# Performance work log

Hardware: AMD Instinct MI355X
Metric: run time of the kernel (lower is better)

## Reference

```python
import jax, jax.numpy as jnp
from jax import lax
import numpy as np
import math

B, H, W = 4, 1080, 1080
MINSIZE = 20
FACTOR = 0.709
THRESH = 0.6
STRIDE = 2.0
CELL = 12.0


def get_scales():
    scales = []
    scale = CELL / MINSIZE
    m = scale * min(H, W)
    while m >= 12:
        scales.append(scale)
        scale *= FACTOR
        m *= FACTOR
    return scales


def setup_inputs() -> dict:
    key = jax.random.key(0)
    ks = jax.random.split(key, 6)
    init = lambda k, shp: jax.random.normal(k, shp, jnp.float32) * 0.1
    return {
        "inputs": jax.random.uniform(ks[0], (B, H, W, 3), jnp.float32) * 255.0,
        "w1": init(ks[1], (3, 3, 3, 10)), "b1": jnp.zeros((10,), jnp.float32),
        "w2": init(ks[2], (3, 3, 10, 16)), "b2": jnp.zeros((16,), jnp.float32),
        "w3": init(ks[3], (3, 3, 16, 32)), "b3": jnp.zeros((32,), jnp.float32),
        "wp": init(ks[4], (1, 1, 32, 2)), "bp": jnp.zeros((2,), jnp.float32),
        "wr": init(ks[5], (1, 1, 32, 4)), "br": jnp.zeros((4,), jnp.float32),
    }


def _conv(x, w, pad):
    return lax.conv_general_dilated(x, w, (1, 1), pad,
                                    dimension_numbers=('NHWC', 'HWIO', 'NHWC'))


def _lrelu(x):
    return jnp.where(x > 0, x, 0.3 * x)  # keras LeakyReLU default alpha=0.3


def _pnet(x, w1, b1, w2, b2, w3, b3, wp, bp, wr, br):
    x = _lrelu(_conv(x, w1, 'VALID') + b1)
    x = lax.reduce_window(x, -jnp.inf, lax.max, (1, 2, 2, 1), (1, 2, 2, 1), 'SAME')
    x = _lrelu(_conv(x, w2, 'VALID') + b2)
    x = _lrelu(_conv(x, w3, 'VALID') + b3)
    probs = jax.nn.softmax(_conv(x, wp, 'SAME') + bp, axis=-1)
    reg = _conv(x, wr, 'SAME') + br
    return probs, reg


def reference(inputs, w1, b1, w2, b2, w3, b3, wp, bp, wr, br):
    boxes_all, reg_all, mask_all = [], [], []
    b = inputs.shape[0]
    for scale in get_scales():
        hs, ws = int(math.ceil(H * scale)), int(math.ceil(W * scale))
        img = (jax.image.resize(inputs, (b, hs, ws, 3), 'bilinear') - 127.5) / 128.0
        probs, reg = _pnet(img, w1, b1, w2, b2, w3, b3, wp, bp, wr, br)
        score = probs[..., 1]  # [B, h, w]
        _, h, w = score.shape
        rr, cc = jnp.meshgrid(jnp.arange(h, dtype=jnp.float32),
                              jnp.arange(w, dtype=jnp.float32), indexing='ij')
        pos = jnp.stack([rr, cc], axis=-1)  # grid positions (row, col)
        ul = jnp.round((pos * STRIDE + 1.0) / scale)          # upper-left corner
        dr = jnp.round((pos * STRIDE + CELL - 1.0 + 1.0) / scale)  # down-right corner
        boxes = jnp.concatenate([
            jnp.broadcast_to(ul, (b, h, w, 2)),
            jnp.broadcast_to(dr, (b, h, w, 2)),
            score[..., None]], axis=-1)  # [B, h, w, 5]
        boxes_all.append(boxes.reshape(b, h * w, 5))
        reg_all.append(reg.reshape(b, h * w, 4))
        mask_all.append((score >= THRESH).reshape(b, h * w))  # rows getBBox would gather
    return (jnp.concatenate(boxes_all, axis=1),
            jnp.concatenate(reg_all, axis=1),
            jnp.concatenate(mask_all, axis=1))
```

## Files before the change

### kernel.cpp

```cpp
#include <hip/hip_runtime.h>
#include <math.h>

#define TPB 256

struct SP {
    int  n;
    int  blkBase[13];
    int  xBase[13];
    int  hs[12];
    int  ph[12];
    int  istr[12];
    int  wstr[12];
    float inv[12];
    float rinv[12];
    float scl[12];
    long wOff[12];
    long jOff[12];
    long tmpOff[12];
    long imgOff[12];
    long pOff[12];
    long qOff[12];
    long base[12];
};

__device__ __forceinline__ float lrelu(float x) { return x > 0.f ? x : 0.3f * x; }

__device__ __forceinline__ int find_scale(const SP& p, int bb) {
    int s = 0;
#pragma unroll
    for (int k = 1; k < 12; k++)
        if (k < p.n && bb >= p.blkBase[k]) s = k;
    return s;
}

__global__ __launch_bounds__(TPB) void k_wt(float* __restrict__ wsb, SP p) {
    int s = blockIdx.x;
    int hs = p.hs[s];
    int wstr = p.wstr[s];
    float inv = p.inv[s], rinv = p.rinv[s];
    float* wt = wsb + p.wOff[s];
    int* jt = (int*)wsb + p.jOff[s];
    for (int x = threadIdx.x; x < hs; x += TPB) {
        float c = ((float)x + 0.5f) * inv - 0.5f;
        int jlo = (int)floorf(c - inv);
        if (jlo < 0) jlo = 0;
        if (jlo > 1080 - wstr) jlo = 1080 - wstr;
        float sum = 0.f;
        for (int k = 0; k < wstr; k++) {
            float w = fmaxf(0.f, 1.f - fabsf(c - (float)(jlo + k)) * rinv);
            sum += w;
        }
        float rt = 1.f / sum;
        for (int k = 0; k < wstr; k++) {
            float w = fmaxf(0.f, 1.f - fabsf(c - (float)(jlo + k)) * rinv);
            wt[k * hs + x] = w * rt;
        }
        jt[x] = jlo;
    }
}

__global__ __launch_bounds__(TPB) void k_hres1(const float* __restrict__ in,
                                               float* __restrict__ wsb, SP p) {
    __shared__ float row[3240];
    __shared__ float sInv[12], sRinv[12];
    __shared__ int sWstr[12], sXB[13];
    __shared__ long sOff[12];
    int r = blockIdx.x;
    if (threadIdx.x < 12) {
        int s = threadIdx.x;
        if (s < p.n) {
            sInv[s] = p.inv[s];
            sRinv[s] = p.rinv[s];
            sWstr[s] = p.wstr[s];
            sXB[s] = p.xBase[s];
            sOff[s] = p.tmpOff[s] + (long)r * p.istr[s];
        }
    }
    if (threadIdx.x == 0) sXB[p.n] = p.xBase[p.n];
    const float4* src = (const float4*)(in + (long)r * 3240);
    float4* row4 = (float4*)row;
    for (int ch = threadIdx.x; ch < 810; ch += TPB) row4[ch] = src[ch];
    __syncthreads();
    int xTot = p.xBase[p.n];
    for (int ft = threadIdx.x; ft < xTot; ft += TPB) {
        int s = 0;
#pragma unroll
        for (int k = 1; k < 12; k++)
            if (k < p.n && ft >= sXB[k]) s = k;
        int x = ft - sXB[s];
        float inv = sInv[s], rinv = sRinv[s];
        int wstr = sWstr[s];
        float c = ((float)x + 0.5f) * inv - 0.5f;
        int jlo = (int)floorf(c - inv);
        if (jlo < 0) jlo = 0;
        int jmax = 1080 - wstr;
        if (jlo > jmax) jlo = jmax;
        float d = c - (float)jlo;
        const float* pr = row + jlo * 3;
        float n0 = 0.f, n1 = 0.f, n2 = 0.f, tw = 0.f;
        for (int k = 0; k < wstr; k++) {
            float w = fmaxf(0.f, fmaf(-fabsf(d), rinv, 1.f));
            tw += w;
            n0 += w * pr[0]; n1 += w * pr[1]; n2 += w * pr[2];
            d -= 1.f; pr += 3;
        }
        float rt = 1.f / tw;
        float* o = wsb + sOff[s] + x * 3;
        o[0] = n0 * rt;
        o[1] = n1 * rt;
        o[2] = n2 * rt;
    }
}

__global__ __launch_bounds__(TPB) void k_vres2(float* __restrict__ wsb, SP p) {
    __shared__ float wsm[152];
    int bb = blockIdx.x;
    int s = find_scale(p, bb);
    int hs = p.hs[s];
    int istr = p.istr[s];
    int wstr = p.wstr[s];
    int r = bb - p.blkBase[s];
    int i = r % hs;
    int b = r / hs;
    int jlo = ((const int*)wsb + p.jOff[s])[i];
    const float* wt = wsb + p.wOff[s];
    for (int k = threadIdx.x; k < wstr; k += TPB)
        wsm[k] = wt[k * hs + i];
    __syncthreads();
    int W4 = istr >> 2;
    const float4* src0 = (const float4*)(wsb + p.tmpOff[s] + ((long)b * 1080 + jlo) * istr);
    float4* dst = (float4*)(wsb + p.imgOff[s] + (long)r * istr);
    for (int ch = threadIdx.x; ch < W4; ch += TPB) {
        float4 acc = {0.f, 0.f, 0.f, 0.f};
        const float4* sp = src0 + ch;
        for (int k = 0; k < wstr; k++) {
            float w = wsm[k];
            float4 v = sp[(long)k * W4];
            acc.x += w * v.x; acc.y += w * v.y; acc.z += w * v.z; acc.w += w * v.w;
        }
        float4 o;
        o.x = (acc.x - 127.5f) * 0.0078125f;
        o.y = (acc.y - 127.5f) * 0.0078125f;
        o.z = (acc.z - 127.5f) * 0.0078125f;
        o.w = (acc.w - 127.5f) * 0.0078125f;
        dst[ch] = o;
    }
}

__global__ __launch_bounds__(TPB) void k_c1p(float* __restrict__ wsb,
                                             const float* __restrict__ w1,
                                             const float* __restrict__ b1, SP p) {
    int bb = blockIdx.x;
    int s = find_scale(p, bb);
    int hs = p.hs[s];
    int istr = p.istr[s];
    int ph = p.ph[s];
    int t = (bb - p.blkBase[s]) * TPB + threadIdx.x;
    if (t >= 4 * ph * ph) return;
    int px = t % ph;
    int rem = t / ph;
    int pi = rem % ph;
    int b = rem / ph;
    const float* img = wsb + p.imgOff[s] + (long)b * hs * istr;
    int r0 = 2 * pi, c0 = 2 * px;
    float im[4][4][3];
#pragma unroll
    for (int dy = 0; dy < 4; dy++) {
        int r = r0 + dy;
#pragma unroll
        for (int dx = 0; dx < 4; dx++) {
            int cc = c0 + dx;
            if (r < hs && cc < hs) {
                const float* pp = img + (long)r * istr + cc * 3;
                im[dy][dx][0] = pp[0]; im[dy][dx][1] = pp[1]; im[dy][dx][2] = pp[2];
            } else {
                im[dy][dx][0] = 0.f; im[dy][dx][1] = 0.f; im[dy][dx][2] = 0.f;
            }
        }
    }
    int ch = hs - 2;
    bool v01 = (c0 + 1) < ch;
    bool v10 = (r0 + 1) < ch;
    bool v11 = v01 && v10;
    float* P = wsb + p.pOff[s] + (((long)b * ph + pi) * ph + px) * 10;
#pragma unroll 1
    for (int oc = 0; oc < 10; ++oc) {
        float bias = b1[oc];
        float a00 = bias, a01 = bias, a10 = bias, a11 = bias;
#pragma unroll
        for (int ky = 0; ky < 3; ky++)
#pragma unroll
            for (int kx = 0; kx < 3; kx++)
#pragma unroll
                for (int ic = 0; ic < 3; ic++) {
                    float w = w1[((ky * 3 + kx) * 3 + ic) * 10 + oc];
                    a00 += im[ky][kx][ic] * w;
                    a01 += im[ky][kx + 1][ic] * w;
                    a10 += im[ky + 1][kx][ic] * w;
                    a11 += im[ky + 1][kx + 1][ic] * w;
                }
        float mx = lrelu(a00);
        if (v01) mx = fmaxf(mx, lrelu(a01));
        if (v10) mx = fmaxf(mx, lrelu(a10));
        if (v11) mx = fmaxf(mx, lrelu(a11));
        P[oc] = mx;
    }
}

__global__ __launch_bounds__(TPB) void k_c2(float* __restrict__ wsb,
                                            const float* __restrict__ w2,
                                            const float* __restrict__ b2, SP p) {
    int bb = blockIdx.x;
    int s = find_scale(p, bb);
    int ph = p.ph[s];
    int qh = ph - 2;
    int t = (bb - p.blkBase[s]) * TPB + threadIdx.x;
    if (t >= 4 * qh * qh) return;
    int qx = t % qh;
    int rem = t / qh;
    int qi = rem % qh;
    int b = rem / qh;
    const float* P = wsb + p.pOff[s] + (long)b * ph * ph * 10;
    float acc[16];
#pragma unroll
    for (int oc = 0; oc < 16; oc++) acc[oc] = b2[oc];
#pragma unroll 1
    for (int pos = 0; pos < 9; pos++) {
        int ky = pos / 3, kx = pos - ky * 3;
        const float* pp = P + ((long)(qi + ky) * ph + (qx + kx)) * 10;
        float v[10];
#pragma unroll
        for (int h = 0; h < 5; h++) {
            float2 v2 = *(const float2*)(pp + 2 * h);
            v[2 * h] = v2.x; v[2 * h + 1] = v2.y;
        }
#pragma unroll
        for (int ic = 0; ic < 10; ic++)
#pragma unroll
            for (int oc = 0; oc < 16; oc++)
                acc[oc] += v[ic] * w2[(pos * 10 + ic) * 16 + oc];
    }
    float* Q = wsb + p.qOff[s] + (((long)b * qh + qi) * qh + qx) * 16;
    float4* Q4 = (float4*)Q;
#pragma unroll
    for (int h = 0; h < 4; h++) {
        float4 o;
        o.x = lrelu(acc[4 * h + 0]); o.y = lrelu(acc[4 * h + 1]);
        o.z = lrelu(acc[4 * h + 2]); o.w = lrelu(acc[4 * h + 3]);
        Q4[h] = o;
    }
}

__global__ __launch_bounds__(TPB) void k_c3h(float* __restrict__ wsb,
                                             const float* __restrict__ w3,
                                             const float* __restrict__ b3,
                                             const float* __restrict__ wp,
                                             const float* __restrict__ bpb,
                                             const float* __restrict__ wr,
                                             const float* __restrict__ brb,
                                             float* __restrict__ out, long N, SP p) {
    int bb = blockIdx.x;
    int s = find_scale(p, bb);
    int ph = p.ph[s];
    int qh = ph - 2;
    int oh = ph - 4;
    int t = (bb - p.blkBase[s]) * TPB + threadIdx.x;
    if (t >= 4 * oh * oh) return;
    int x = t % oh;
    int rem = t / oh;
    int y = rem % oh;
    int b = rem / oh;
    const float* Q = wsb + p.qOff[s] + (long)b * qh * qh * 16;
    float acc[32];
#pragma unroll
    for (int oc = 0; oc < 32; oc++) acc[oc] = b3[oc];
#pragma unroll 1
    for (int pos = 0; pos < 9; pos++) {
        int ky = pos / 3, kx = pos - ky * 3;
        const float4* qq = (const float4*)(Q + ((long)(y + ky) * qh + (x + kx)) * 16);
        float v[16];
#pragma unroll
        for (int h = 0; h < 4; h++) {
            float4 v4 = qq[h];
            v[4 * h] = v4.x; v[4 * h + 1] = v4.y; v[4 * h + 2] = v4.z; v[4 * h + 3] = v4.w;
        }
#pragma unroll
        for (int ic = 0; ic < 16; ic++)
#pragma unroll
            for (int oc = 0; oc < 32; oc++)
                acc[oc] += v[ic] * w3[(pos * 16 + ic) * 32 + oc];
    }
#pragma unroll
    for (int oc = 0; oc < 32; oc++) acc[oc] = lrelu(acc[oc]);
    float p0 = bpb[0], p1 = bpb[1];
    float r0 = brb[0], r1 = brb[1], r2 = brb[2], r3 = brb[3];
#pragma unroll
    for (int ic = 0; ic < 32; ic++) {
        float v = acc[ic];
        p0 += v * wp[ic * 2 + 0]; p1 += v * wp[ic * 2 + 1];
        r0 += v * wr[ic * 4 + 0]; r1 += v * wr[ic * 4 + 1];
        r2 += v * wr[ic * 4 + 2]; r3 += v * wr[ic * 4 + 3];
    }
    float mx = fmaxf(p0, p1);
    float e0 = expf(p0 - mx), e1 = expf(p1 - mx);
    float score = e1 / (e0 + e1);
    float sclf = p.scl[s];
    long idx = p.base[s] + (long)y * oh + x;
    long g = (long)b * N + idx;
    float fy = (float)y, fx = (float)x;
    float* ob = out + g * 5;
    ob[0] = rintf((2.f * fy + 1.f) / sclf);
    ob[1] = rintf((2.f * fx + 1.f) / sclf);
    ob[2] = rintf((2.f * fy + 12.f) / sclf);
    ob[3] = rintf((2.f * fx + 12.f) / sclf);
    ob[4] = score;
    float* orr = out + N * 20 + g * 4;
    orr[0] = r0; orr[1] = r1; orr[2] = r2; orr[3] = r3;
    out[N * 36 + g] = (score >= 0.6f) ? 1.f : 0.f;
}

static int fill_blocks(SP& q, const int* cnt) {
    int acc = 0;
    for (int s = 0; s < q.n; s++) {
        q.blkBase[s] = acc;
        acc += (cnt[s] + TPB - 1) / TPB;
    }
    q.blkBase[q.n] = acc;
    return acc;
}

static int fill_rows(SP& q, const int* cnt) {
    int acc = 0;
    for (int s = 0; s < q.n; s++) {
        q.blkBase[s] = acc;
        acc += cnt[s];
    }
    q.blkBase[q.n] = acc;
    return acc;
}

extern "C" void kernel_launch(void* const* d_in, const int* in_sizes, int n_in,
                              void* d_out, int out_size, void* d_ws, size_t ws_size,
                              hipStream_t stream) {
    const float* in = (const float*)d_in[0];
    const float* w1 = (const float*)d_in[1];
    const float* b1 = (const float*)d_in[2];
    const float* w2 = (const float*)d_in[3];
    const float* b2 = (const float*)d_in[4];
    const float* w3 = (const float*)d_in[5];
    const float* b3 = (const float*)d_in[6];
    const float* wp = (const float*)d_in[7];
    const float* bp = (const float*)d_in[8];
    const float* wr = (const float*)d_in[9];
    const float* br = (const float*)d_in[10];
    float* ws = (float*)d_ws;
    float* out = (float*)d_out;

    double sc = 12.0 / 20.0, m = sc * 1080.0;
    int ns = 0;
    double scl[12];
    while (m >= 12.0 && ns < 12) { scl[ns++] = sc; sc *= 0.709; m *= 0.709; }

    int hs[12], ph[12], istr[12], wstr[12];
    long base[12];
    long N = 0;
    for (int s = 0; s < ns; s++) {
        hs[s] = (int)ceil(1080.0 * scl[s]);
        ph[s] = (hs[s] - 1) / 2;
        istr[s] = ((hs[s] * 3 + 3) / 4) * 4;
        double invd = 1080.0 / (double)hs[s];
        wstr[s] = (int)ceil(2.0 * invd) + 2;
        if (wstr[s] > 1080) wstr[s] = 1080;
    }
    for (int s = 0; s < ns; s++) {
        int oh = ph[s] - 4;
        base[s] = N;
        N += (long)oh * oh;
    }

    long wOff[12], jOff[12], tmpOff[12], imgOff[12], pOff[12], qOff[12];
    long off = 0;
    for (int s = 0; s < ns; s++) { wOff[s] = off; off += (long)wstr[s] * hs[s]; }
    for (int s = 0; s < ns; s++) { jOff[s] = off; off += hs[s]; }
    off = (off + 3) & ~3L;
    long tabEnd = off;
    for (int s = 0; s < ns; s++) { tmpOff[s] = off; off += 4L * 1080 * istr[s]; }
    for (int s = 0; s < ns; s++) { imgOff[s] = off; off += 4L * hs[s] * istr[s]; }
    for (int s = 0; s < ns; s++) { pOff[s] = off; off += 4L * ph[s] * ph[s] * 10; }
    for (int s = 0; s < ns; s++) { qOff[s] = off; off += 4L * (ph[s] - 2) * (ph[s] - 2) * 16; }
    bool batched = (ws_size >= (size_t)off * 4);
    if (!batched) {
        long TMP2MAX = 4L * 1080 * istr[0];
        long IMGMAX = 4L * hs[0] * istr[0];
        long PMAX = 4L * ph[0] * ph[0] * 10;
        for (int s = 0; s < ns; s++) {
            tmpOff[s] = tabEnd;
            imgOff[s] = tabEnd + TMP2MAX;
            pOff[s] = tabEnd + TMP2MAX + IMGMAX;
            qOff[s] = tabEnd + TMP2MAX + IMGMAX + PMAX;
        }
    }

    SP pAll;
    pAll.n = ns;
    for (int s = 0; s < ns; s++) {
        pAll.hs[s] = hs[s]; pAll.ph[s] = ph[s]; pAll.istr[s] = istr[s];
        pAll.wstr[s] = wstr[s];
        pAll.inv[s] = (float)(1080.0 / (double)hs[s]);
        pAll.rinv[s] = (float)((double)hs[s] / 1080.0);
        pAll.scl[s] = (float)scl[s];
        pAll.wOff[s] = wOff[s]; pAll.jOff[s] = jOff[s];
        pAll.tmpOff[s] = tmpOff[s]; pAll.imgOff[s] = imgOff[s];
        pAll.pOff[s] = pOff[s]; pAll.qOff[s] = qOff[s];
        pAll.base[s] = base[s];
    }
    k_wt<<<ns, TPB, 0, stream>>>(ws, pAll);

    int gcount = batched ? 1 : ns;
    for (int g = 0; g < gcount; ++g) {
        int s0 = batched ? 0 : g;
        int cnt = batched ? ns : 1;
        SP p;
        p.n = cnt;
        int xacc = 0;
        for (int k = 0; k < cnt; k++) {
            int s = s0 + k;
            p.hs[k] = hs[s]; p.ph[k] = ph[s]; p.istr[k] = istr[s];
            p.wstr[k] = wstr[s];
            p.xBase[k] = xacc; xacc += hs[s];
            p.inv[k] = (float)(1080.0 / (double)hs[s]);
            p.rinv[k] = (float)((double)hs[s] / 1080.0);
            p.scl[k] = (float)scl[s];
            p.wOff[k] = wOff[s]; p.jOff[k] = jOff[s];
            p.tmpOff[k] = tmpOff[s]; p.imgOff[k] = imgOff[s];
            p.pOff[k] = pOff[s]; p.qOff[k] = qOff[s];
            p.base[k] = base[s];
        }
        p.xBase[cnt] = xacc;
        int crow[12], c3[12], c4[12], c5[12];
        for (int k = 0; k < cnt; k++) {
            int s = s0 + k;
            int PH = ph[s], QH = PH - 2, OH = PH - 4;
            crow[k] = 4 * hs[s];
            c3[k] = 4 * PH * PH;
            c4[k] = 4 * QH * QH;
            c5[k] = 4 * OH * OH;
        }
        int nb;
        SP ps = p;
        k_hres1<<<4 * 1080, TPB, 0, stream>>>(in, ws, p);
        ps = p; nb = fill_rows(ps, crow);
        k_vres2<<<nb, TPB, 0, stream>>>(ws, ps);
        ps = p; nb = fill_blocks(ps, c3);
        k_c1p<<<nb, TPB, 0, stream>>>(ws, w1, b1, ps);
        ps = p; nb = fill_blocks(ps, c4);
        k_c2<<<nb, TPB, 0, stream>>>(ws, w2, b2, ps);
        ps = p; nb = fill_blocks(ps, c5);
        k_c3h<<<nb, TPB, 0, stream>>>(ws, w3, b3, wp, bp, wr, br, out, N, ps);
    }
}
```

Before: 445.8 us.

## Register-block conv2 into 2x2 outputs and conv3 into 1x2 outputs per thread

Conv2 now computes a 2x2 patch of output pixels per thread, loading a 4x4 input window once and reusing each weight across four accumulators. Conv3 plus the head computes two horizontally adjacent outputs per thread, sharing column loads and weight reads. The goal is to cut redundant global/L1 loads and weight fetches per FLOP. In exchange, register pressure rises (64 and 64+ accumulators), which may lower occupancy or cause spills, and fewer threads are launched.

```diff
diff --git a/kernel.cpp b/kernel.cpp
--- a/kernel.cpp
+++ b/kernel.cpp
@@ -214,41 +214,126 @@
     int s = find_scale(p, bb);
     int ph = p.ph[s];
     int qh = ph - 2;
+    int qhx = (qh + 1) >> 1;
     int t = (bb - p.blkBase[s]) * TPB + threadIdx.x;
-    if (t >= 4 * qh * qh) return;
-    int qx = t % qh;
-    int rem = t / qh;
-    int qi = rem % qh;
-    int b = rem / qh;
+    if (t >= 4 * qhx * qhx) return;
+    int qxt = t % qhx;
+    int rem = t / qhx;
+    int qyt = rem % qhx;
+    int b = rem / qhx;
+    int qx = 2 * qxt, qy = 2 * qyt;
+    bool vx = (qx + 1) < qh, vy = (qy + 1) < qh;
     const float* P = wsb + p.pOff[s] + (long)b * ph * ph * 10;
-    float acc[16];
-#pragma unroll
-    for (int oc = 0; oc < 16; oc++) acc[oc] = b2[oc];
+    float acc[4][16];
+#pragma unroll
+    for (int oc = 0; oc < 16; oc++) {
+        float bv = b2[oc];
+        acc[0][oc] = bv; acc[1][oc] = bv; acc[2][oc] = bv; acc[3][oc] = bv;
+    }
 #pragma unroll 1
-    for (int pos = 0; pos < 9; pos++) {
-        int ky = pos / 3, kx = pos - ky * 3;
-        const float* pp = P + ((long)(qi + ky) * ph + (qx + kx)) * 10;
-        float v[10];
-#pragma unroll
-        for (int h = 0; h < 5; h++) {
-            float2 v2 = *(const float2*)(pp + 2 * h);
-            v[2 * h] = v2.x; v[2 * h + 1] = v2.y;
-        }
-#pragma unroll
-        for (int ic = 0; ic < 10; ic++)
-#pragma unroll
-            for (int oc = 0; oc < 16; oc++)
-                acc[oc] += v[ic] * w2[(pos * 10 + ic) * 16 + oc];
-    }
-    float* Q = wsb + p.qOff[s] + (((long)b * qh + qi) * qh + qx) * 16;
-    float4* Q4 = (float4*)Q;
+    for (int ky = 0; ky < 4; ky++) {
+        int rr = qy + ky; if (rr > ph - 1) rr = ph - 1;
+        const float* rowp = P + (long)rr * ph * 10;
+        float pix[4][10];
+#pragma unroll
+        for (int ci = 0; ci < 4; ci++) {
+            int cc = qx + ci; if (cc > ph - 1) cc = ph - 1;
+            const float2* pp = (const float2*)(rowp + cc * 10);
+#pragma unroll
+            for (int h = 0; h < 5; h++) {
+                float2 v2 = pp[h];
+                pix[ci][2 * h] = v2.x; pix[ci][2 * h + 1] = v2.y;
+            }
+        }
+        if (ky <= 2) {
+            int pos0 = ky * 3;
+#pragma unroll
+            for (int kx = 0; kx < 3; kx++)
+#pragma unroll
+                for (int ic = 0; ic < 10; ic++)
+#pragma unroll
+                    for (int oc = 0; oc < 16; oc++) {
+                        float w = w2[((pos0 + kx) * 10 + ic) * 16 + oc];
+                        acc[0][oc] += pix[kx][ic] * w;
+                        acc[1][oc] += pix[kx + 1][ic] * w;
+                    }
+        }
+        if (ky >= 1) {
+            int pos0 = (ky - 1) * 3;
+#pragma unroll
+            for (int kx = 0; kx < 3; kx++)
+#pragma unroll
+                for (int ic = 0; ic < 10; ic++)
+#pragma unroll
+                    for (int oc = 0; oc < 16; oc++) {
+                        float w = w2[((pos0 + kx) * 10 + ic) * 16 + oc];
+                        acc[2][oc] += pix[kx][ic] * w;
+                        acc[3][oc] += pix[kx + 1][ic] * w;
+                    }
+        }
+    }
+    float* Qb = wsb + p.qOff[s] + (long)b * qh * qh * 16;
+#pragma unroll
+    for (int oy = 0; oy < 2; oy++) {
+#pragma unroll
+        for (int ox = 0; ox < 2; ox++) {
+            if ((oy == 1 && !vy) || (ox == 1 && !vx)) continue;
+            float4* Q4 = (float4*)(Qb + ((long)(qy + oy) * qh + (qx + ox)) * 16);
+            const float* a = acc[oy * 2 + ox];
+#pragma unroll
+            for (int h = 0; h < 4; h++) {
+                float4 o;
+                o.x = lrelu(a[4 * h + 0]); o.y = lrelu(a[4 * h + 1]);
+                o.z = lrelu(a[4 * h + 2]); o.w = lrelu(a[4 * h + 3]);
+                Q4[h] = o;
+            }
+        }
+    }
+}
+
+__device__ __forceinline__ void ldcol16(float v[16], const float* q) {
 #pragma unroll
     for (int h = 0; h < 4; h++) {
-        float4 o;
-        o.x = lrelu(acc[4 * h + 0]); o.y = lrelu(acc[4 * h + 1]);
-        o.z = lrelu(acc[4 * h + 2]); o.w = lrelu(acc[4 * h + 3]);
-        Q4[h] = o;
-    }
+        float4 t4 = ((const float4*)q)[h];
+        v[4 * h] = t4.x; v[4 * h + 1] = t4.y; v[4 * h + 2] = t4.z; v[4 * h + 3] = t4.w;
+    }
+}
+
+__device__ __forceinline__ void mac32(float acc[32], const float v[16],
+                                      const float* __restrict__ w3, int pos) {
+#pragma unroll
+    for (int ic = 0; ic < 16; ic++)
+#pragma unroll
+        for (int oc = 0; oc < 32; oc++)
+            acc[oc] += v[ic] * w3[(pos * 16 + ic) * 32 + oc];
+}
+
+__device__ __forceinline__ void head_store(const float acc[32],
+                                           const float* __restrict__ wp, const float* __restrict__ bpb,
+                                           const float* __restrict__ wr, const float* __restrict__ brb,
+                                           float* __restrict__ out, long N, long g,
+                                           float sclf, float fy, float fx) {
+    float p0 = bpb[0], p1 = bpb[1];
+    float r0 = brb[0], r1 = brb[1], r2 = brb[2], r3 = brb[3];
+#pragma unroll
+    for (int ic = 0; ic < 32; ic++) {
+        float v = lrelu(acc[ic]);
+        p0 += v * wp[ic * 2 + 0]; p1 += v * wp[ic * 2 + 1];
+        r0 += v * wr[ic * 4 + 0]; r1 += v * wr[ic * 4 + 1];
+        r2 += v * wr[ic * 4 + 2]; r3 += v * wr[ic * 4 + 3];
+    }
+    float mx = fmaxf(p0, p1);
+    float e0 = expf(p0 - mx), e1 = expf(p1 - mx);
+    float score = e1 / (e0 + e1);
+    float* ob = out + g * 5;
+    ob[0] = rintf((2.f * fy + 1.f) / sclf);
+    ob[1] = rintf((2.f * fx + 1.f) / sclf);
+    ob[2] = rintf((2.f * fy + 12.f) / sclf);
+    ob[3] = rintf((2.f * fx + 12.f) / sclf);
+    ob[4] = score;
+    float* orr = out + N * 20 + g * 4;
+    orr[0] = r0; orr[1] = r1; orr[2] = r2; orr[3] = r3;
+    out[N * 36 + g] = (score >= 0.6f) ? 1.f : 0.f;
 }
 
 __global__ __launch_bounds__(TPB) void k_c3h(float* __restrict__ wsb,
@@ -264,59 +349,39 @@
     int ph = p.ph[s];
     int qh = ph - 2;
     int oh = ph - 4;
+    int ohx = (oh + 1) >> 1;
     int t = (bb - p.blkBase[s]) * TPB + threadIdx.x;
-    if (t >= 4 * oh * oh) return;
-    int x = t % oh;
-    int rem = t / oh;
+    if (t >= 4 * oh * ohx) return;
+    int xt = t % ohx;
+    int rem = t / ohx;
     int y = rem % oh;
     int b = rem / oh;
+    int x = 2 * xt;
+    bool vx = (x + 1) < oh;
     const float* Q = wsb + p.qOff[s] + (long)b * qh * qh * 16;
-    float acc[32];
-#pragma unroll
-    for (int oc = 0; oc < 32; oc++) acc[oc] = b3[oc];
+    float acc0[32], acc1[32];
+#pragma unroll
+    for (int oc = 0; oc < 32; oc++) { float bv = b3[oc]; acc0[oc] = bv; acc1[oc] = bv; }
 #pragma unroll 1
-    for (int pos = 0; pos < 9; pos++) {
-        int ky = pos / 3, kx = pos - ky * 3;
-        const float4* qq = (const float4*)(Q + ((long)(y + ky) * qh + (x + kx)) * 16);
-        float v[16];
-#pragma unroll
-        for (int h = 0; h < 4; h++) {
-            float4 v4 = qq[h];
-            v[4 * h] = v4.x; v[4 * h + 1] = v4.y; v[4 * h + 2] = v4.z; v[4 * h + 3] = v4.w;
-        }
-#pragma unroll
-        for (int ic = 0; ic < 16; ic++)
-#pragma unroll
-            for (int oc = 0; oc < 32; oc++)
-                acc[oc] += v[ic] * w3[(pos * 16 + ic) * 32 + oc];
-    }
-#pragma unroll
-    for (int oc = 0; oc < 32; oc++) acc[oc] = lrelu(acc[oc]);
-    float p0 = bpb[0], p1 = bpb[1];
-    float r0 = brb[0], r1 = brb[1], r2 = brb[2], r3 = brb[3];
-#pragma unroll
-    for (int ic = 0; ic < 32; ic++) {
-        float v = acc[ic];
-        p0 += v * wp[ic * 2 + 0]; p1 += v * wp[ic * 2 + 1];
-        r0 += v * wr[ic * 4 + 0]; r1 += v * wr[ic * 4 + 1];
-        r2 += v * wr[ic * 4 + 2]; r3 += v * wr[ic * 4 + 3];
-    }
-    float mx = fmaxf(p0, p1);
-    float e0 = expf(p0 - mx), e1 = expf(p1 - mx);
-    float score = e1 / (e0 + e1);
+    for (int ky = 0; ky < 3; ky++) {
+        const float* rowp = Q + (long)(y + ky) * qh * 16;
+        int c3i = x + 3; if (c3i > qh - 1) c3i = qh - 1;
+        float ca[16], cb[16];
+        ldcol16(ca, rowp + (long)x * 16);
+        ldcol16(cb, rowp + (long)(x + 1) * 16);
+        int pos = ky * 3;
+        mac32(acc0, ca, w3, pos);     mac32(acc1, cb, w3, pos);
+        ldcol16(ca, rowp + (long)(x + 2) * 16);
+        mac32(acc0, cb, w3, pos + 1); mac32(acc1, ca, w3, pos + 1);
+        ldcol16(cb, rowp + (long)c3i * 16);
+        mac32(acc0, ca, w3, pos + 2); mac32(acc1, cb, w3, pos + 2);
+    }
     float sclf = p.scl[s];
     long idx = p.base[s] + (long)y * oh + x;
     long g = (long)b * N + idx;
-    float fy = (float)y, fx = (float)x;
-    float* ob = out + g * 5;
-    ob[0] = rintf((2.f * fy + 1.f) / sclf);
-    ob[1] = rintf((2.f * fx + 1.f) / sclf);
-    ob[2] = rintf((2.f * fy + 12.f) / sclf);
-    ob[3] = rintf((2.f * fx + 12.f) / sclf);
-    ob[4] = score;
-    float* orr = out + N * 20 + g * 4;
-    orr[0] = r0; orr[1] = r1; orr[2] = r2; orr[3] = r3;
-    out[N * 36 + g] = (score >= 0.6f) ? 1.f : 0.f;
+    head_store(acc0, wp, bpb, wr, brb, out, N, g, sclf, (float)y, (float)x);
+    if (vx)
+        head_store(acc1, wp, bpb, wr, brb, out, N, g + 1, sclf, (float)y, (float)(x + 1));
 }
 
 static int fill_blocks(SP& q, const int* cnt) {
@@ -441,10 +506,11 @@
         for (int k = 0; k < cnt; k++) {
             int s = s0 + k;
             int PH = ph[s], QH = PH - 2, OH = PH - 4;
+            int QHX = (QH + 1) / 2, OHX = (OH + 1) / 2;
             crow[k] = 4 * hs[s];
             c3[k] = 4 * PH * PH;
-            c4[k] = 4 * QH * QH;
-            c5[k] = 4 * OH * OH;
+            c4[k] = 4 * QHX * QHX;
+            c5[k] = 4 * OH * OHX;
         }
         int nb;
         SP ps = p;
```

Measured after the change: 459.3 us. 3.0% more time.

## Tile conv3 head kernel into 16x16 output blocks with shared-memory halo staging

Applied to the files above, without the earlier changes.

The conv3+head kernel now assigns one block per 16x16 output tile per image and scale. Before computing, the block cooperatively copies an 18x18 halo of the 16-channel conv2 output into LDS, padded to 20 floats per site. The 9 taps then read from LDS rather than re-reading global memory for each neighbouring pixel. The cost is a sync barrier, idle threads on partial edge tiles (noticeable at the small scales), and higher LDS use per block, which may reduce occupancy.

```diff
diff --git a/kernel.cpp b/kernel.cpp
--- a/kernel.cpp
+++ b/kernel.cpp
@@ -2,6 +2,7 @@
 #include <math.h>
 
 #define TPB 256
+#define C3T 16
 
 struct SP {
     int  n;
@@ -259,29 +260,43 @@
                                              const float* __restrict__ wr,
                                              const float* __restrict__ brb,
                                              float* __restrict__ out, long N, SP p) {
+    __shared__ float Qs[18 * 18 * 20];
     int bb = blockIdx.x;
     int s = find_scale(p, bb);
     int ph = p.ph[s];
     int qh = ph - 2;
     int oh = ph - 4;
-    int t = (bb - p.blkBase[s]) * TPB + threadIdx.x;
-    if (t >= 4 * oh * oh) return;
-    int x = t % oh;
-    int rem = t / oh;
-    int y = rem % oh;
-    int b = rem / oh;
+    int ntx = (oh + C3T - 1) / C3T;
+    int tile = bb - p.blkBase[s];
+    int tx = tile % ntx;
+    int rem = tile / ntx;
+    int ty = rem % ntx;
+    int b = rem / ntx;
+    int x0 = tx * C3T, y0 = ty * C3T;
     const float* Q = wsb + p.qOff[s] + (long)b * qh * qh * 16;
+    for (int site = threadIdx.x; site < 324; site += TPB) {
+        int lr = site / 18, lc = site - lr * 18;
+        int gr = y0 + lr; if (gr > qh - 1) gr = qh - 1;
+        int gc = x0 + lc; if (gc > qh - 1) gc = qh - 1;
+        const float4* srcp = (const float4*)(Q + ((long)gr * qh + gc) * 16);
+        float4* dstp = (float4*)&Qs[(lr * 18 + lc) * 20];
+#pragma unroll
+        for (int h = 0; h < 4; h++) dstp[h] = srcp[h];
+    }
+    __syncthreads();
+    int ox = threadIdx.x & 15, oy = threadIdx.x >> 4;
+    int x = x0 + ox, y = y0 + oy;
     float acc[32];
 #pragma unroll
     for (int oc = 0; oc < 32; oc++) acc[oc] = b3[oc];
 #pragma unroll 1
     for (int pos = 0; pos < 9; pos++) {
         int ky = pos / 3, kx = pos - ky * 3;
-        const float4* qq = (const float4*)(Q + ((long)(y + ky) * qh + (x + kx)) * 16);
+        const float4* cp = (const float4*)&Qs[((oy + ky) * 18 + ox + kx) * 20];
         float v[16];
 #pragma unroll
         for (int h = 0; h < 4; h++) {
-            float4 v4 = qq[h];
+            float4 v4 = cp[h];
             v[4 * h] = v4.x; v[4 * h + 1] = v4.y; v[4 * h + 2] = v4.z; v[4 * h + 3] = v4.w;
         }
 #pragma unroll
@@ -290,13 +305,12 @@
             for (int oc = 0; oc < 32; oc++)
                 acc[oc] += v[ic] * w3[(pos * 16 + ic) * 32 + oc];
     }
-#pragma unroll
-    for (int oc = 0; oc < 32; oc++) acc[oc] = lrelu(acc[oc]);
+    if (x >= oh || y >= oh) return;
     float p0 = bpb[0], p1 = bpb[1];
     float r0 = brb[0], r1 = brb[1], r2 = brb[2], r3 = brb[3];
 #pragma unroll
     for (int ic = 0; ic < 32; ic++) {
-        float v = acc[ic];
+        float v = lrelu(acc[ic]);
         p0 += v * wp[ic * 2 + 0]; p1 += v * wp[ic * 2 + 1];
         r0 += v * wr[ic * 4 + 0]; r1 += v * wr[ic * 4 + 1];
         r2 += v * wr[ic * 4 + 2]; r3 += v * wr[ic * 4 + 3];
@@ -441,10 +455,11 @@
         for (int k = 0; k < cnt; k++) {
             int s = s0 + k;
             int PH = ph[s], QH = PH - 2, OH = PH - 4;
+            int NTX = (OH + C3T - 1) / C3T;
             crow[k] = 4 * hs[s];
             c3[k] = 4 * PH * PH;
             c4[k] = 4 * QH * QH;
-            c5[k] = 4 * OH * OH;
+            c5[k] = 4 * NTX * NTX;
         }
         int nb;
         SP ps = p;
@@ -455,7 +470,7 @@
         k_c1p<<<nb, TPB, 0, stream>>>(ws, w1, b1, ps);
         ps = p; nb = fill_blocks(ps, c4);
         k_c2<<<nb, TPB, 0, stream>>>(ws, w2, b2, ps);
-        ps = p; nb = fill_blocks(ps, c5);
+        ps = p; nb = fill_rows(ps, c5);
         k_c3h<<<nb, TPB, 0, stream>>>(ws, w3, b3, wp, bp, wr, br, out, N, ps);
     }
 }
```

Measured after the change: 431.9 us. -3.1%, faster.
